# Kernel tuning notes

Measured on AMD Instinct MI355X. Metric: run time of the kernel, lower is better.

The kernel has to match this reference:

```python
import jax, jax.numpy as jnp
import numpy as np

N_EMBD = 1024
HEAD_SIZE = 64
B, T = 16, 2048


def setup_inputs() -> dict:
    key = jax.random.key(0)
    ks = jax.random.split(key, 7)
    s = 1.0 / np.sqrt(N_EMBD)
    return {
        "x": jax.random.normal(ks[0], (B, T, N_EMBD), dtype=jnp.float32),
        "Wq": jax.random.uniform(ks[1], (N_EMBD, HEAD_SIZE), jnp.float32, -s, s),
        "bq": jax.random.uniform(ks[2], (HEAD_SIZE,), jnp.float32, -s, s),
        "Wk": jax.random.uniform(ks[3], (N_EMBD, HEAD_SIZE), jnp.float32, -s, s),
        "bk": jax.random.uniform(ks[4], (HEAD_SIZE,), jnp.float32, -s, s),
        "Wv": jax.random.uniform(ks[5], (N_EMBD, HEAD_SIZE), jnp.float32, -s, s),
        "bv": jax.random.uniform(ks[6], (HEAD_SIZE,), jnp.float32, -s, s),
    }


def reference(x, Wq, bq, Wk, bk, Wv, bv):
    # x: [B, T, C]
    q = x @ Wq + bq          # [B, T, H]
    k = x @ Wk + bk          # [B, T, H]
    v = x @ Wv + bv          # [B, T, H]
    scale = k.shape[-1] ** -0.5
    wei = jnp.einsum("bth,bsh->bts", q, k) * scale  # [B, T, T]
    Tn = x.shape[1]
    causal = jnp.tril(jnp.ones((Tn, Tn), dtype=bool))
    wei = jnp.where(causal, wei, -jnp.inf)
    wei = jax.nn.softmax(wei, axis=-1)
    # dropout is identity in eval mode
    return jnp.einsum("bts,bsh->bth", wei, v)  # [B, T, H]
```

## Files before the change

kernel.cpp:

```cpp
#include <hip/hip_runtime.h>
#include <math.h>

#define BB 16
#define TT 2048
#define CC 1024
#define HH 64
#define MTOT (BB*TT)

typedef _Float16 f16;
typedef _Float16 f16x4 __attribute__((ext_vector_type(4)));
typedef _Float16 f16x8 __attribute__((ext_vector_type(8)));
typedef float f32x4 __attribute__((ext_vector_type(4)));

#define WT_OFF 0
#define Q_OFF  196608
#define K_OFF  (Q_OFF + (size_t)MTOT*HH)
#define VT_OFF (K_OFF + (size_t)MTOT*HH)

__device__ __forceinline__ void async16(const void* g, void* l) {
    __builtin_amdgcn_global_load_lds(
        (const __attribute__((address_space(1))) unsigned int*)g,
        (__attribute__((address_space(3))) unsigned int*)l, 16, 0, 0);
}

__device__ __forceinline__ f16x8 cvt8(float4 u, float4 v) {
    f16x8 r;
    r[0] = (f16)u.x; r[1] = (f16)u.y; r[2] = (f16)u.z; r[3] = (f16)u.w;
    r[4] = (f16)v.x; r[5] = (f16)v.y; r[6] = (f16)v.z; r[7] = (f16)v.w;
    return r;
}

__global__ __launch_bounds__(256) void prep_kernel(
    const float* __restrict__ Wq, const float* __restrict__ Wk,
    const float* __restrict__ Wv, f16* __restrict__ ws)
{
    int e = blockIdx.x * 256 + threadIdx.x;
    int ng = e >> 10, k = e & 1023;
    int which = ng >> 6, n = ng & 63;
    const float* W = (which == 0) ? Wq : (which == 1) ? Wk : Wv;
    ws[WT_OFF + e] = (f16)W[k * HH + n];
}

__global__ __launch_bounds__(256, 3) void qkv_kernel(
    const float* __restrict__ x,
    const float* __restrict__ bq, const float* __restrict__ bk,
    const float* __restrict__ bv, f16* __restrict__ ws)
{
    __shared__ __align__(16) float Xs[64 * 64];
    __shared__ __align__(16) f16   Ws[192 * 64];
    f16 (*Vt)[72] = (f16 (*)[72])Xs;

    const f16* wt = ws + WT_OFF;
    const int tid  = threadIdx.x;
    const int lane = tid & 63, w = tid >> 6;
    const int c = lane & 15, g = lane >> 4;
    const int m0 = blockIdx.x * 64;

    f32x4 acc[4][3];
    #pragma unroll
    for (int mt = 0; mt < 4; ++mt)
        #pragma unroll
        for (int j = 0; j < 3; ++j) acc[mt][j] = (f32x4){0.f, 0.f, 0.f, 0.f};

    for (int k0 = 0; k0 < CC; k0 += 64) {
        __syncthreads();
        #pragma unroll
        for (int i = 0; i < 4; ++i) {
            int G0 = (w * 4 + i) * 64;
            int G = G0 + lane;
            int r = G >> 4, q = G & 15;
            async16(x + (size_t)(m0 + r) * CC + k0 + ((q ^ (r & 15)) << 2),
                    Xs + G0 * 4);
        }
        #pragma unroll
        for (int i = 0; i < 6; ++i) {
            int G0 = (w * 6 + i) * 64;
            int G = G0 + lane;
            int r = G >> 3, q = G & 7;
            async16(wt + (size_t)r * CC + k0 + ((q ^ (r & 7)) << 3),
                    Ws + G0 * 8);
        }
        __syncthreads();

        #pragma unroll
        for (int kk = 0; kk < 2; ++kk) {
            f16x8 bfr[3];
            #pragma unroll
            for (int j = 0; j < 3; ++j) {
                int r = (3 * w + j) * 16 + c;
                int p = (kk * 4 + g) ^ (c & 7);
                bfr[j] = *(const f16x8*)(Ws + r * 64 + p * 8);
            }
            #pragma unroll
            for (int mt = 0; mt < 4; ++mt) {
                int r = mt * 16 + c;
                int q = kk * 8 + 2 * g;
                float4 f0 = *(const float4*)(Xs + r * 64 + (q ^ c) * 4);
                float4 f1 = *(const float4*)(Xs + r * 64 + ((q + 1) ^ c) * 4);
                f16x8 a = cvt8(f0, f1);
                #pragma unroll
                for (int j = 0; j < 3; ++j)
                    acc[mt][j] = __builtin_amdgcn_mfma_f32_16x16x32_f16(
                        a, bfr[j], acc[mt][j], 0, 0, 0);
            }
        }
    }
    __syncthreads();

    #pragma unroll
    for (int j = 0; j < 3; ++j) {
        int nt = 3 * w + j;
        int plane = nt >> 2;
        int h = (nt & 3) * 16 + c;
        if (plane == 0) {
            float bias = bq[h];
            #pragma unroll
            for (int mt = 0; mt < 4; ++mt)
                #pragma unroll
                for (int r = 0; r < 4; ++r) {
                    int m = m0 + mt * 16 + 4 * g + r;
                    ws[Q_OFF + (size_t)m * HH + h] =
                        (f16)((acc[mt][j][r] + bias) * 0.125f);
                }
        } else if (plane == 1) {
            float bias = bk[h];
            #pragma unroll
            for (int mt = 0; mt < 4; ++mt)
                #pragma unroll
                for (int r = 0; r < 4; ++r) {
                    int m = m0 + mt * 16 + 4 * g + r;
                    ws[K_OFF + (size_t)m * HH + h] = (f16)(acc[mt][j][r] + bias);
                }
        } else {
            float bias = bv[h];
            #pragma unroll
            for (int mt = 0; mt < 4; ++mt)
                #pragma unroll
                for (int r = 0; r < 4; ++r)
                    Vt[h][mt * 16 + 4 * g + r] = (f16)(acc[mt][j][r] + bias);
        }
    }
    __syncthreads();
    {
        int h = tid >> 2, seg = tid & 3;
        f16* dst = ws + VT_OFF + (size_t)h * MTOT + m0 + seg * 16;
        *(f16x8*)dst       = *(f16x8*)&Vt[h][seg * 16];
        *(f16x8*)(dst + 8) = *(f16x8*)&Vt[h][seg * 16 + 8];
    }
}

__global__ __launch_bounds__(256, 3) void attn_kernel(
    const f16* __restrict__ ws, float* __restrict__ out)
{
    const f16* qp = ws + Q_OFF;
    const f16* kp = ws + K_OFF;
    const f16* vt = ws + VT_OFF;

    __shared__ __align__(16) f16 Ks[2][64 * 64];
    __shared__ __align__(16) f16 Vs[2][64 * 64];
    __shared__ __align__(16) f16 PsT[4][16][68];

    const int tid  = threadIdx.x;
    const int lane = tid & 63, w = tid >> 6;
    const int c = lane & 15, g = lane >> 4;

    const int id = blockIdx.x;
    const int r8 = id & 7, j = id >> 3;
    const int half = j >> 5, qr = j & 31;
    const int b  = 2 * r8 + half;
    const int qi = half ? (31 - qr) : qr;
    const int q0 = qi * 64;
    const size_t rowbase = (size_t)b * TT;

    f16x8 bq_[2];
    {
        const f16* qrow = qp + (rowbase + q0 + w * 16 + c) * HH + g * 8;
        bq_[0] = *(const f16x8*)(qrow);
        bq_[1] = *(const f16x8*)(qrow + 32);
    }

    f32x4 o[4];
    #pragma unroll
    for (int ht = 0; ht < 4; ++ht) o[ht] = (f32x4){0.f, 0.f, 0.f, 0.f};
    float l_acc = 0.f;

    #define STAGE_KV(st) do {                                              \
        int buf = (st) & 1;                                                \
        _Pragma("unroll")                                                  \
        for (int i = 0; i < 2; ++i) {                                      \
            int G0 = (w * 2 + i) * 64;                                     \
            int G = G0 + lane;                                             \
            int r = G >> 3, q = G & 7;                                     \
            int sw = (q ^ (r & 7)) << 3;                                   \
            async16(kp + (rowbase + (st) * 64 + r) * HH + sw, &Ks[buf][G0 * 8]); \
            async16(vt + (size_t)r * MTOT + rowbase + (st) * 64 + sw, &Vs[buf][G0 * 8]); \
        }                                                                  \
    } while (0)

    STAGE_KV(0);

    for (int st = 0; st <= qi; ++st) {
        __syncthreads();
        if (st < qi) STAGE_KV(st + 1);
        const f16* kb = Ks[st & 1];
        const f16* vb = Vs[st & 1];
        const int tmax = (st == qi) ? w : 3;
        const bool diag = (st == qi);

        float lp = 0.f;
        #pragma unroll
        for (int t = 0; t < 4; ++t) {
            f16x4 pv;
            if (t <= tmax) {
                int r = t * 16 + c;
                f16x8 a0 = *(const f16x8*)(kb + r * 64 + (((g)     ^ (c & 7)) << 3));
                f16x8 a1 = *(const f16x8*)(kb + r * 64 + (((4 + g) ^ (c & 7)) << 3));
                f32x4 s = (f32x4){0.f, 0.f, 0.f, 0.f};
                s = __builtin_amdgcn_mfma_f32_16x16x32_f16(a0, bq_[0], s, 0, 0, 0);
                s = __builtin_amdgcn_mfma_f32_16x16x32_f16(a1, bq_[1], s, 0, 0, 0);
                #pragma unroll
                for (int rr = 0; rr < 4; ++rr) {
                    float p = (diag && t == w && (4 * g + rr > c))
                                ? 0.f : __expf(s[rr]);
                    lp += p;
                    pv[rr] = (f16)p;
                }
            } else {
                pv = (f16x4){(f16)0.f, (f16)0.f, (f16)0.f, (f16)0.f};
            }
            *(f16x4*)&PsT[w][c][t * 16 + 4 * g] = pv;
        }
        lp += __shfl_xor(lp, 16);
        lp += __shfl_xor(lp, 32);
        l_acc += lp;

        f16x8 pb0 = *(const f16x8*)&PsT[w][c][g * 8];
        f16x8 pb1 = *(const f16x8*)&PsT[w][c][32 + g * 8];
        #pragma unroll
        for (int ht = 0; ht < 4; ++ht) {
            int r = ht * 16 + c;
            f16x8 va0 = *(const f16x8*)(vb + r * 64 + (((g)     ^ (c & 7)) << 3));
            f16x8 va1 = *(const f16x8*)(vb + r * 64 + (((4 + g) ^ (c & 7)) << 3));
            o[ht] = __builtin_amdgcn_mfma_f32_16x16x32_f16(va0, pb0, o[ht], 0, 0, 0);
            o[ht] = __builtin_amdgcn_mfma_f32_16x16x32_f16(va1, pb1, o[ht], 0, 0, 0);
        }
    }
    #undef STAGE_KV

    float inv = 1.0f / l_acc;
    float* orow = out + (rowbase + q0 + w * 16 + c) * HH;
    #pragma unroll
    for (int ht = 0; ht < 4; ++ht) {
        float4 v;
        v.x = o[ht][0] * inv; v.y = o[ht][1] * inv;
        v.z = o[ht][2] * inv; v.w = o[ht][3] * inv;
        *(float4*)(orow + ht * 16 + 4 * g) = v;
    }
}

extern "C" void kernel_launch(void* const* d_in, const int* in_sizes, int n_in,
                              void* d_out, int out_size, void* d_ws, size_t ws_size,
                              hipStream_t stream) {
    const float* x  = (const float*)d_in[0];
    const float* Wq = (const float*)d_in[1];
    const float* bq = (const float*)d_in[2];
    const float* Wk = (const float*)d_in[3];
    const float* bk = (const float*)d_in[4];
    const float* Wv = (const float*)d_in[5];
    const float* bv = (const float*)d_in[6];
    f16*   ws  = (f16*)d_ws;
    float* out = (float*)d_out;

    prep_kernel<<<768, 256, 0, stream>>>(Wq, Wk, Wv, ws);
    qkv_kernel<<<MTOT / 64, 256, 0, stream>>>(x, bq, bk, bv, ws);
    attn_kernel<<<512, 256, 0, stream>>>(ws, out);
}
```

Baseline: 245.5 us.

## Double-buffer QKV projection and halve attention query tile per block

The projection kernel now stages 32-wide K slices into double-buffered LDS with new swizzles, so the next slice's async loads overlap the current MFMA work. The attention kernel moves to 128-thread blocks covering 32 query rows each, launching 1024 blocks for finer causal load balance, with a per-row diagonal mask. Folding log2(e) into the Q scale lets exp2f replace __expf. The risks are extra barriers per K step and more redundant K/V staging across the smaller attention blocks.

```diff
diff --git a/kernel.cpp b/kernel.cpp
--- a/kernel.cpp
+++ b/kernel.cpp
@@ -16,6 +16,8 @@
 #define Q_OFF  196608
 #define K_OFF  (Q_OFF + (size_t)MTOT*HH)
 #define VT_OFF (K_OFF + (size_t)MTOT*HH)
+
+#define QSCALE 0.18033688011112042f
 
 __device__ __forceinline__ void async16(const void* g, void* l) {
     __builtin_amdgcn_global_load_lds(
@@ -41,13 +43,13 @@
     ws[WT_OFF + e] = (f16)W[k * HH + n];
 }
 
-__global__ __launch_bounds__(256, 3) void qkv_kernel(
+__global__ __launch_bounds__(256, 2) void qkv_kernel(
     const float* __restrict__ x,
     const float* __restrict__ bq, const float* __restrict__ bk,
     const float* __restrict__ bv, f16* __restrict__ ws)
 {
-    __shared__ __align__(16) float Xs[64 * 64];
-    __shared__ __align__(16) f16   Ws[192 * 64];
+    __shared__ __align__(16) float Xs[2][64 * 32];
+    __shared__ __align__(16) f16   Ws[2][192 * 32];
     f16 (*Vt)[72] = (f16 (*)[72])Xs;
 
     const f16* wt = ws + WT_OFF;
@@ -62,49 +64,58 @@
         #pragma unroll
         for (int j = 0; j < 3; ++j) acc[mt][j] = (f32x4){0.f, 0.f, 0.f, 0.f};
 
-    for (int k0 = 0; k0 < CC; k0 += 64) {
+    #define STAGE(it) do {                                                  \
+        int buf = (it) & 1;                                                 \
+        int k0 = (it) * 32;                                                 \
+        _Pragma("unroll")                                                   \
+        for (int i = 0; i < 2; ++i) {           \
+            int G0 = (w * 2 + i) * 64;                                      \
+            int G = G0 + lane;                                              \
+            int r = G >> 3, qs = G & 7;                                     \
+            int qg = qs ^ (r & 7);                                          \
+            async16(x + (size_t)(m0 + r) * CC + k0 + qg * 4,                \
+                    &Xs[buf][G0 * 4]);                                      \
+        }                                                                   \
+        _Pragma("unroll")                                                   \
+        for (int i = 0; i < 3; ++i) {            \
+            int G0 = (w * 3 + i) * 64;                                      \
+            int G = G0 + lane;                                              \
+            int r = G >> 2, qs = G & 3;                                     \
+            int qg = qs ^ ((r ^ (r >> 2)) & 3);                             \
+            async16(wt + (size_t)r * CC + k0 + qg * 8,                      \
+                    &Ws[buf][G0 * 8]);                                      \
+        }                                                                   \
+    } while (0)
+
+    STAGE(0);
+
+    #pragma unroll 2
+    for (int it = 0; it < 32; ++it) {
         __syncthreads();
-        #pragma unroll
-        for (int i = 0; i < 4; ++i) {
-            int G0 = (w * 4 + i) * 64;
-            int G = G0 + lane;
-            int r = G >> 4, q = G & 15;
-            async16(x + (size_t)(m0 + r) * CC + k0 + ((q ^ (r & 15)) << 2),
-                    Xs + G0 * 4);
-        }
-        #pragma unroll
-        for (int i = 0; i < 6; ++i) {
-            int G0 = (w * 6 + i) * 64;
-            int G = G0 + lane;
-            int r = G >> 3, q = G & 7;
-            async16(wt + (size_t)r * CC + k0 + ((q ^ (r & 7)) << 3),
-                    Ws + G0 * 8);
-        }
-        __syncthreads();
-
-        #pragma unroll
-        for (int kk = 0; kk < 2; ++kk) {
-            f16x8 bfr[3];
-            #pragma unroll
-            for (int j = 0; j < 3; ++j) {
-                int r = (3 * w + j) * 16 + c;
-                int p = (kk * 4 + g) ^ (c & 7);
-                bfr[j] = *(const f16x8*)(Ws + r * 64 + p * 8);
-            }
-            #pragma unroll
-            for (int mt = 0; mt < 4; ++mt) {
-                int r = mt * 16 + c;
-                int q = kk * 8 + 2 * g;
-                float4 f0 = *(const float4*)(Xs + r * 64 + (q ^ c) * 4);
-                float4 f1 = *(const float4*)(Xs + r * 64 + ((q + 1) ^ c) * 4);
-                f16x8 a = cvt8(f0, f1);
-                #pragma unroll
-                for (int j = 0; j < 3; ++j)
-                    acc[mt][j] = __builtin_amdgcn_mfma_f32_16x16x32_f16(
-                        a, bfr[j], acc[mt][j], 0, 0, 0);
-            }
-        }
-    }
+        if (it < 31) STAGE(it + 1);
+        const float* xb = Xs[it & 1];
+        const f16*   wb = Ws[it & 1];
+
+        f16x8 bfr[3];
+        #pragma unroll
+        for (int j = 0; j < 3; ++j) {
+            int r = (3 * w + j) * 16 + c;
+            int pos = g ^ ((c ^ (c >> 2)) & 3);
+            bfr[j] = *(const f16x8*)(wb + r * 32 + pos * 8);
+        }
+        #pragma unroll
+        for (int mt = 0; mt < 4; ++mt) {
+            int r = mt * 16 + c;
+            float4 f0 = *(const float4*)(xb + r * 32 + (((2 * g)     ^ (c & 7)) * 4));
+            float4 f1 = *(const float4*)(xb + r * 32 + (((2 * g + 1) ^ (c & 7)) * 4));
+            f16x8 a = cvt8(f0, f1);
+            #pragma unroll
+            for (int j = 0; j < 3; ++j)
+                acc[mt][j] = __builtin_amdgcn_mfma_f32_16x16x32_f16(
+                    a, bfr[j], acc[mt][j], 0, 0, 0);
+        }
+    }
+    #undef STAGE
     __syncthreads();
 
     #pragma unroll
@@ -120,7 +131,7 @@
                 for (int r = 0; r < 4; ++r) {
                     int m = m0 + mt * 16 + 4 * g + r;
                     ws[Q_OFF + (size_t)m * HH + h] =
-                        (f16)((acc[mt][j][r] + bias) * 0.125f);
+                        (f16)((acc[mt][j][r] + bias) * QSCALE);
                 }
         } else if (plane == 1) {
             float bias = bk[h];
@@ -149,7 +160,7 @@
     }
 }
 
-__global__ __launch_bounds__(256, 3) void attn_kernel(
+__global__ __launch_bounds__(128, 2) void attn_kernel(
     const f16* __restrict__ ws, float* __restrict__ out)
 {
     const f16* qp = ws + Q_OFF;
@@ -158,7 +169,7 @@
 
     __shared__ __align__(16) f16 Ks[2][64 * 64];
     __shared__ __align__(16) f16 Vs[2][64 * 64];
-    __shared__ __align__(16) f16 PsT[4][16][68];
+    __shared__ __align__(16) f16 PsT[2][16][72];
 
     const int tid  = threadIdx.x;
     const int lane = tid & 63, w = tid >> 6;
@@ -166,10 +177,10 @@
 
     const int id = blockIdx.x;
     const int r8 = id & 7, j = id >> 3;
-    const int half = j >> 5, qr = j & 31;
+    const int half = j >> 6, qr = j & 63;
     const int b  = 2 * r8 + half;
-    const int qi = half ? (31 - qr) : qr;
-    const int q0 = qi * 64;
+    const int qi = half ? (63 - qr) : qr;
+    const int q0 = qi * 32;
     const size_t rowbase = (size_t)b * TT;
 
     f16x8 bq_[2];
@@ -187,25 +198,27 @@
     #define STAGE_KV(st) do {                                              \
         int buf = (st) & 1;                                                \
         _Pragma("unroll")                                                  \
-        for (int i = 0; i < 2; ++i) {                                      \
-            int G0 = (w * 2 + i) * 64;                                     \
+        for (int i = 0; i < 4; ++i) {                                      \
+            int G0 = (w * 4 + i) * 64;                                     \
             int G = G0 + lane;                                             \
-            int r = G >> 3, q = G & 7;                                     \
-            int sw = (q ^ (r & 7)) << 3;                                   \
+            int r = G >> 3, qs = G & 7;                                    \
+            int sw = (qs ^ (r & 7)) << 3;                                  \
             async16(kp + (rowbase + (st) * 64 + r) * HH + sw, &Ks[buf][G0 * 8]); \
             async16(vt + (size_t)r * MTOT + rowbase + (st) * 64 + sw, &Vs[buf][G0 * 8]); \
         }                                                                  \
     } while (0)
 
+    const int nst = (qi >> 1) + 1;
     STAGE_KV(0);
 
-    for (int st = 0; st <= qi; ++st) {
+    for (int st = 0; st < nst; ++st) {
         __syncthreads();
-        if (st < qi) STAGE_KV(st + 1);
+        if (st + 1 < nst) STAGE_KV(st + 1);
         const f16* kb = Ks[st & 1];
         const f16* vb = Vs[st & 1];
-        const int tmax = (st == qi) ? w : 3;
-        const bool diag = (st == qi);
+        const bool diag = (st == nst - 1);
+        const int tmax = diag ? (w + 2 * (qi & 1)) : 3;
+        const int rel  = q0 + 16 * w + c - st * 64;
 
         float lp = 0.f;
         #pragma unroll
@@ -220,8 +233,8 @@
                 s = __builtin_amdgcn_mfma_f32_16x16x32_f16(a1, bq_[1], s, 0, 0, 0);
                 #pragma unroll
                 for (int rr = 0; rr < 4; ++rr) {
-                    float p = (diag && t == w && (4 * g + rr > c))
-                                ? 0.f : __expf(s[rr]);
+                    float p = (diag && (t * 16 + 4 * g + rr > rel))
+                                ? 0.f : exp2f(s[rr]);
                     lp += p;
                     pv[rr] = (f16)p;
                 }
@@ -273,5 +286,5 @@
 
     prep_kernel<<<768, 256, 0, stream>>>(Wq, Wk, Wv, ws);
     qkv_kernel<<<MTOT / 64, 256, 0, stream>>>(x, bq, bk, bv, ws);
-    attn_kernel<<<512, 256, 0, stream>>>(ws, out);
-}
+    attn_kernel<<<1024, 128, 0, stream>>>(ws, out);
+}
```

New measurement: 265.0 us. 1.08x slower.
